# Performance work log

Measured on AMD Instinct MI355X. Metric: run time of the kernel, lower is better.

Reference implementation:

```python
import jax, jax.numpy as jnp
import numpy as np

N, L, E, H, D = 4, 2048, 1024, 16, 64

def setup_inputs() -> dict:
    key = jax.random.key(0)
    ks = jax.random.split(key, 8)
    s = 1.0 / np.sqrt(E)
    return {
        "Q": jax.random.normal(ks[0], (N, L, E), jnp.float32),
        "K": jax.random.normal(ks[1], (N, L, E), jnp.float32),
        "V": jax.random.normal(ks[2], (N, L, E), jnp.float32),
        "Wq": jax.random.normal(ks[3], (H * D, E), jnp.float32) * s,
        "bq": jnp.zeros((H * D,), jnp.float32),
        "Wk": jax.random.normal(ks[4], (H * D, E), jnp.float32) * s,
        "bk": jnp.zeros((H * D,), jnp.float32),
        "Wv": jax.random.normal(ks[5], (H * D, E), jnp.float32) * s,
        "bv": jnp.zeros((H * D,), jnp.float32),
        "Wo": jax.random.normal(ks[6], (E, H * D), jnp.float32) * s,
        "bo": jnp.zeros((E,), jnp.float32),
    }

def reference(Q, K, V, Wq, bq, Wk, bk, Wv, bv, Wo, bo):
    n, lq, e = Q.shape
    lk = K.shape[1]
    # projections: Linear(x) = x @ W.T + b
    q = (Q @ Wq.T + bq).reshape(n, lq, H, D)
    k = (K @ Wk.T + bk).reshape(n, lk, H, D)
    v = (V @ Wv.T + bv).reshape(n, lk, H, D)
    # scores over key dim (original broadcasts Q*K and sums over d)
    scores = jnp.einsum('nqhd,nkhd->nqkh', q, k) / jnp.sqrt(jnp.float32(D))
    attn = jax.nn.softmax(scores, axis=2)  # softmax over key axis
    out = jnp.einsum('nqkh,nkhd->nqhd', attn, v)
    out = out.reshape(n, lq, H * D)
    return (out @ Wo.T + bo).reshape(n, lq, E)
```

## Files before the change

kernel.cpp:

```cpp
#include <hip/hip_runtime.h>
#include <cstdint>
#include <cstddef>


typedef __bf16 bf16x8 __attribute__((ext_vector_type(8)));
typedef __bf16 bf16x4 __attribute__((ext_vector_type(4)));
typedef float f32x4 __attribute__((ext_vector_type(4)));

#define LOG2E_OVER_SQRTD 0.18033688011112042f

__device__ __forceinline__ unsigned short f2bf(float f) {
  unsigned int u = __builtin_bit_cast(unsigned int, f);
  u = (u + 0x7fffu + ((u >> 16) & 1u)) >> 16;
  return (unsigned short)u;
}

__device__ __forceinline__ void gl2lds16(const void* g, void* l) {
  __builtin_amdgcn_global_load_lds(
      (__attribute__((address_space(1))) unsigned int*)g,
      (__attribute__((address_space(3))) unsigned int*)l, 16, 0, 0);
}

struct CvtArgs {
  const float* src[4];
  unsigned short* dst[4];
};
__global__ __launch_bounds__(256) void cvt_multi_k(CvtArgs a) {
  const float* s = a.src[blockIdx.y];
  unsigned short* d = a.dst[blockIdx.y];
  size_t i = ((size_t)blockIdx.x * 256 + threadIdx.x) * 4;
  float4 v = *(const float4*)(s + i);
  ushort4 o;
  o.x = f2bf(v.x); o.y = f2bf(v.y); o.z = f2bf(v.z); o.w = f2bf(v.w);
  *(ushort4*)(d + i) = o;
}

template <bool OUT_F32, bool BIAS_ROW, bool PERMC>
__global__ __launch_bounds__(256, 2) void gemm_bt_k(
    const unsigned short* __restrict__ A, const unsigned short* __restrict__ Bt,
    const float* __restrict__ bias, void* __restrict__ Cv, int M, int N,
    float out_scale) {
  __shared__ __attribute__((aligned(16))) unsigned short As[128 * 32];
  __shared__ __attribute__((aligned(16))) unsigned short Bs[128 * 32];
  const int tid = threadIdx.x;
  const int lane = tid & 63, wave = tid >> 6;
  const int lr = lane & 15, lg = lane >> 4;
  const int rowBase = blockIdx.y * 128;
  const int colBase = blockIdx.x * 128;
  const int wm = (wave & 1) * 64, wn = (wave >> 1) * 64;

  f32x4 acc[4][4] = {};

  const int s0 = tid, s1 = tid + 256;
  const int r0 = s0 >> 2, c0 = (s0 & 3) ^ ((r0 >> 1) & 3);
  const int r1 = s1 >> 2, c1 = (s1 & 3) ^ ((r1 >> 1) & 3);
  const unsigned short* gA0 = A + (size_t)(rowBase + r0) * 1024 + c0 * 8;
  const unsigned short* gA1 = A + (size_t)(rowBase + r1) * 1024 + c1 * 8;
  const unsigned short* gB0 = Bt + (size_t)(colBase + r0) * 1024 + c0 * 8;
  const unsigned short* gB1 = Bt + (size_t)(colBase + r1) * 1024 + c1 * 8;
  unsigned short* lA0 = &As[s0 * 8];
  unsigned short* lA1 = &As[s1 * 8];
  unsigned short* lB0 = &Bs[s0 * 8];
  unsigned short* lB1 = &Bs[s1 * 8];

  for (int kt = 0; kt < 32; ++kt) {
    gl2lds16(gA0 + kt * 32, lA0);
    gl2lds16(gA1 + kt * 32, lA1);
    gl2lds16(gB0 + kt * 32, lB0);
    gl2lds16(gB1 + kt * 32, lB1);
    __syncthreads();

    bf16x8 af[4], bfr[4];
#pragma unroll
    for (int mt = 0; mt < 4; ++mt) {
      int row = wm + mt * 16 + lr;
      int seg = lg ^ ((row >> 1) & 3);
      af[mt] = *(const bf16x8*)&As[row * 32 + seg * 8];
    }
#pragma unroll
    for (int nt = 0; nt < 4; ++nt) {
      int row = wn + nt * 16 + lr;
      int seg = lg ^ ((row >> 1) & 3);
      bfr[nt] = *(const bf16x8*)&Bs[row * 32 + seg * 8];
    }
#pragma unroll
    for (int mt = 0; mt < 4; ++mt)
#pragma unroll
      for (int nt = 0; nt < 4; ++nt)
        acc[mt][nt] = __builtin_amdgcn_mfma_f32_16x16x32_bf16(
            af[mt], bfr[nt], acc[mt][nt], 0, 0, 0);
    __syncthreads();
  }

#pragma unroll
  for (int mt = 0; mt < 4; ++mt)
#pragma unroll
    for (int nt = 0; nt < 4; ++nt) {
      int col = colBase + wn + nt * 16 + lr;
      int colStore = PERMC ? (colBase + wn + lr * 4 + nt) : col;
      float bcol = BIAS_ROW ? 0.f : bias[col];
#pragma unroll
      for (int r = 0; r < 4; ++r) {
        int row = rowBase + wm + mt * 16 + lg * 4 + r;
        float b = BIAS_ROW ? bias[row] : bcol;
        float val = (acc[mt][nt][r] + b) * out_scale;
        size_t idx = (size_t)row * (size_t)N + (size_t)colStore;
        if (OUT_F32)
          ((float*)Cv)[idx] = val;
        else
          ((unsigned short*)Cv)[idx] = f2bf(val);
      }
    }
}

__global__ __launch_bounds__(256, 4) void attn_k(
    const unsigned short* __restrict__ qb,
    const unsigned short* __restrict__ kb,
    const unsigned short* __restrict__ vtb,
    unsigned short* __restrict__ aob) {
  __shared__ __attribute__((aligned(16))) unsigned short Ks[64 * 64];
  __shared__ __attribute__((aligned(16))) unsigned short Vts[64 * 64];
  __shared__ __attribute__((aligned(16))) unsigned short QPs[4 * 32 * 72];

  const int tid = threadIdx.x;
  const int lane = tid & 63, wave = tid >> 6;
  const int lr = lane & 15, lg = lane >> 4;

  const int bid = blockIdx.x;
  const int qt = bid & 15;
  const int nh = bid >> 4;
  const int h = nh & 15, n = nh >> 4;
  const int q0 = qt * 128;

#pragma unroll
  for (int i = 0; i < 4; ++i) {
    int s = i * 256 + tid;
    int row = s >> 3;
    int c = (s & 7) ^ (row & 7);
    gl2lds16(qb + (((size_t)n * 2048 + q0 + row) << 10) + h * 64 + c * 8,
             &QPs[s * 8]);
  }
#pragma unroll
  for (int i = 0; i < 2; ++i) {
    int s = i * 256 + tid;
    int row = s >> 3;
    int c = (s & 7) ^ (row & 7);
    gl2lds16(kb + (((size_t)n * 2048 + row) << 10) + h * 64 + c * 8, &Ks[s * 8]);
    gl2lds16(vtb + (((size_t)(h * 64 + row)) << 13) + (size_t)n * 2048 + c * 8,
             &Vts[s * 8]);
  }
  __syncthreads();

  bf16x8 aq[2][2];
#pragma unroll
  for (int mt = 0; mt < 2; ++mt)
#pragma unroll
    for (int ks = 0; ks < 2; ++ks) {
      int row = wave * 32 + mt * 16 + lr;
      int c = (ks * 4 + lg) ^ (row & 7);
      aq[mt][ks] = *(const bf16x8*)&QPs[row * 64 + c * 8];
    }
  __syncthreads();

  unsigned short* PsW = &QPs[wave * (32 * 72)];

  f32x4 o_acc[2][4] = {};
  float lrow[2][4] = {};

  for (int kt = 0; kt < 32; ++kt) {
    f32x4 s_acc[2][4] = {};
#pragma unroll
    for (int ks = 0; ks < 2; ++ks)
#pragma unroll
      for (int nt = 0; nt < 4; ++nt) {
        int row = nt * 16 + lr;
        int c = (ks * 4 + lg) ^ (row & 7);
        bf16x8 bk = *(const bf16x8*)&Ks[row * 64 + c * 8];
#pragma unroll
        for (int mt = 0; mt < 2; ++mt)
          s_acc[mt][nt] = __builtin_amdgcn_mfma_f32_16x16x32_bf16(
              aq[mt][ks], bk, s_acc[mt][nt], 0, 0, 0);
      }

#pragma unroll
    for (int mt = 0; mt < 2; ++mt) {
      f32x4 p[4];
#pragma unroll
      for (int nt = 0; nt < 4; ++nt)
#pragma unroll
        for (int r = 0; r < 4; ++r)
          p[nt][r] = __builtin_amdgcn_exp2f(s_acc[mt][nt][r]);
#pragma unroll
      for (int r = 0; r < 4; ++r) {
        lrow[mt][r] += (p[0][r] + p[1][r]) + (p[2][r] + p[3][r]);
        f32x4 v4 = {p[0][r], p[1][r], p[2][r], p[3][r]};
        bf16x4 pk = __builtin_convertvector(v4, bf16x4);
        int prow = mt * 16 + lg * 4 + r;
        *(bf16x4*)&PsW[prow * 72 + lr * 4] = pk;
      }
    }

#pragma unroll
    for (int ks = 0; ks < 2; ++ks) {
      bf16x8 ap[2], bv[4];
#pragma unroll
      for (int mt = 0; mt < 2; ++mt)
        ap[mt] = *(const bf16x8*)&PsW[(mt * 16 + lr) * 72 + ks * 32 + lg * 8];
#pragma unroll
      for (int nt = 0; nt < 4; ++nt) {
        int row = nt * 16 + lr;
        int c = (ks * 4 + lg) ^ (row & 7);
        bv[nt] = *(const bf16x8*)&Vts[row * 64 + c * 8];
      }
#pragma unroll
      for (int mt = 0; mt < 2; ++mt)
#pragma unroll
        for (int nt = 0; nt < 4; ++nt)
          o_acc[mt][nt] = __builtin_amdgcn_mfma_f32_16x16x32_bf16(
              ap[mt], bv[nt], o_acc[mt][nt], 0, 0, 0);
    }

    __syncthreads();
    if (kt < 31) {
      const int k0 = (kt + 1) * 64;
#pragma unroll
      for (int i = 0; i < 2; ++i) {
        int s = i * 256 + tid;
        int row = s >> 3;
        int c = (s & 7) ^ (row & 7);
        gl2lds16(kb + (((size_t)n * 2048 + k0 + row) << 10) + h * 64 + c * 8,
                 &Ks[s * 8]);
        gl2lds16(vtb + (((size_t)(h * 64 + row)) << 13) + (size_t)n * 2048 +
                     k0 + c * 8,
                 &Vts[s * 8]);
      }
    }
    __syncthreads();
  }

#pragma unroll
  for (int mt = 0; mt < 2; ++mt)
#pragma unroll
    for (int r = 0; r < 4; ++r) {
      float l = lrow[mt][r];
      l += __shfl_xor(l, 1);
      l += __shfl_xor(l, 2);
      l += __shfl_xor(l, 4);
      l += __shfl_xor(l, 8);
      float inv = 1.0f / l;
      int row_l = q0 + wave * 32 + mt * 16 + lg * 4 + r;
      size_t base = (((size_t)n * 2048 + row_l) << 10) + h * 64;
#pragma unroll
      for (int nt = 0; nt < 4; ++nt)
        aob[base + nt * 16 + lr] = f2bf(o_acc[mt][nt][r] * inv);
    }
}

extern "C" void kernel_launch(void* const* d_in, const int* in_sizes, int n_in,
                              void* d_out, int out_size, void* d_ws,
                              size_t ws_size, hipStream_t stream) {
  const float* Q = (const float*)d_in[0];
  const float* K = (const float*)d_in[1];
  const float* V = (const float*)d_in[2];
  const float* Wq = (const float*)d_in[3];
  const float* bq = (const float*)d_in[4];
  const float* Wk = (const float*)d_in[5];
  const float* bk = (const float*)d_in[6];
  const float* Wv = (const float*)d_in[7];
  const float* bv = (const float*)d_in[8];
  const float* Wo = (const float*)d_in[9];
  const float* bo = (const float*)d_in[10];

  const size_t S = (size_t)8192 * 1024;
  const size_t W = (size_t)1024 * 1024;
  unsigned short* ws = (unsigned short*)d_ws;
  unsigned short* Qbf = ws;
  unsigned short* Kbf = ws + S;
  unsigned short* Vbf = ws + 2 * S;
  unsigned short* qbuf = ws + 3 * S;
  unsigned short* kbuf = ws + 4 * S;
  unsigned short* vtbuf = ws + 5 * S;
  unsigned short* Wqb = ws + 6 * S;
  unsigned short* Wkb = Wqb + W;
  unsigned short* Wvb = Wqb + 2 * W;
  unsigned short* Wob = Wqb + 3 * W;
  unsigned short* aob = Qbf;

  CvtArgs cx;
  cx.src[0] = Q; cx.dst[0] = Qbf;
  cx.src[1] = K; cx.dst[1] = Kbf;
  cx.src[2] = V; cx.dst[2] = Vbf;
  cx.src[3] = Q; cx.dst[3] = Qbf;
  cvt_multi_k<<<dim3(8192, 3), 256, 0, stream>>>(cx);

  CvtArgs cw;
  cw.src[0] = Wq; cw.dst[0] = Wqb;
  cw.src[1] = Wk; cw.dst[1] = Wkb;
  cw.src[2] = Wv; cw.dst[2] = Wvb;
  cw.src[3] = Wo; cw.dst[3] = Wob;
  cvt_multi_k<<<dim3(1024, 4), 256, 0, stream>>>(cw);

  gemm_bt_k<false, false, false><<<dim3(8, 64), 256, 0, stream>>>(
      Qbf, Wqb, bq, qbuf, 8192, 1024, LOG2E_OVER_SQRTD);
  gemm_bt_k<false, false, false><<<dim3(8, 64), 256, 0, stream>>>(
      Kbf, Wkb, bk, kbuf, 8192, 1024, 1.0f);
  gemm_bt_k<false, true, true><<<dim3(64, 8), 256, 0, stream>>>(
      Wvb, Vbf, bv, vtbuf, 1024, 8192, 1.0f);

  attn_k<<<1024, 256, 0, stream>>>(qbuf, kbuf, vtbuf, aob);

  gemm_bt_k<true, false, false><<<dim3(8, 64), 256, 0, stream>>>(
      aob, Wob, bo, d_out, 8192, 1024, 1.0f);
}
```

Measured before the change: 353.5 us.

## Batch Q/K/V projection GEMMs into one launch and deepen K tile to 64

Merges the three projection GEMMs into a single grouped launch of 1536 blocks, with a descriptor table picking the operands for each block. This lets the three GEMMs fill the GPU together and removes per-launch tail effects. The K tile per iteration grows from 32 to 64, which halves the number of barrier-synchronised loads and uses an 8-way XOR swizzle. In exchange, LDS per block doubles to 32KB, and bias/permute choices become runtime branches instead of template specialisations.

```diff
diff --git a/kernel.cpp b/kernel.cpp
--- a/kernel.cpp
+++ b/kernel.cpp
@@ -35,60 +35,85 @@
   *(ushort4*)(d + i) = o;
 }
 
-template <bool OUT_F32, bool BIAS_ROW, bool PERMC>
-__global__ __launch_bounds__(256, 2) void gemm_bt_k(
-    const unsigned short* __restrict__ A, const unsigned short* __restrict__ Bt,
-    const float* __restrict__ bias, void* __restrict__ Cv, int M, int N,
-    float out_scale) {
-  __shared__ __attribute__((aligned(16))) unsigned short As[128 * 32];
-  __shared__ __attribute__((aligned(16))) unsigned short Bs[128 * 32];
+struct GemmDesc {
+  const unsigned short* A;
+  const unsigned short* Bt;
+  const float* bias;
+  void* C;
+  int N;
+  int nbx_shift;
+  float scale;
+  int bias_row;
+  int permc;
+};
+struct GemmPack3 {
+  GemmDesc g[3];
+};
+
+template <bool OUT_F32>
+__global__ __launch_bounds__(256, 2) void gemm_multi_k(GemmPack3 p) {
+  __shared__ __attribute__((aligned(16))) unsigned short As[128 * 64];
+  __shared__ __attribute__((aligned(16))) unsigned short Bs[128 * 64];
+  const GemmDesc d = p.g[blockIdx.x >> 9];
+  const int t = blockIdx.x & 511;
+  const int bx = t & ((1 << d.nbx_shift) - 1);
+  const int by = t >> d.nbx_shift;
+
   const int tid = threadIdx.x;
   const int lane = tid & 63, wave = tid >> 6;
   const int lr = lane & 15, lg = lane >> 4;
-  const int rowBase = blockIdx.y * 128;
-  const int colBase = blockIdx.x * 128;
+  const int rowBase = by * 128;
+  const int colBase = bx * 128;
   const int wm = (wave & 1) * 64, wn = (wave >> 1) * 64;
 
   f32x4 acc[4][4] = {};
 
-  const int s0 = tid, s1 = tid + 256;
-  const int r0 = s0 >> 2, c0 = (s0 & 3) ^ ((r0 >> 1) & 3);
-  const int r1 = s1 >> 2, c1 = (s1 & 3) ^ ((r1 >> 1) & 3);
-  const unsigned short* gA0 = A + (size_t)(rowBase + r0) * 1024 + c0 * 8;
-  const unsigned short* gA1 = A + (size_t)(rowBase + r1) * 1024 + c1 * 8;
-  const unsigned short* gB0 = Bt + (size_t)(colBase + r0) * 1024 + c0 * 8;
-  const unsigned short* gB1 = Bt + (size_t)(colBase + r1) * 1024 + c1 * 8;
-  unsigned short* lA0 = &As[s0 * 8];
-  unsigned short* lA1 = &As[s1 * 8];
-  unsigned short* lB0 = &Bs[s0 * 8];
-  unsigned short* lB1 = &Bs[s1 * 8];
-
-  for (int kt = 0; kt < 32; ++kt) {
-    gl2lds16(gA0 + kt * 32, lA0);
-    gl2lds16(gA1 + kt * 32, lA1);
-    gl2lds16(gB0 + kt * 32, lB0);
-    gl2lds16(gB1 + kt * 32, lB1);
+  const unsigned short* gA[4];
+  const unsigned short* gB[4];
+  unsigned short* lA[4];
+  unsigned short* lB[4];
+#pragma unroll
+  for (int i = 0; i < 4; ++i) {
+    int s = tid + i * 256;
+    int row = s >> 3;
+    int c = (s & 7) ^ (row & 7);
+    gA[i] = d.A + (size_t)(rowBase + row) * 1024 + c * 8;
+    gB[i] = d.Bt + (size_t)(colBase + row) * 1024 + c * 8;
+    lA[i] = &As[s * 8];
+    lB[i] = &Bs[s * 8];
+  }
+
+  for (int kt = 0; kt < 16; ++kt) {
+    const int ko = kt * 64;
+#pragma unroll
+    for (int i = 0; i < 4; ++i) {
+      gl2lds16(gA[i] + ko, lA[i]);
+      gl2lds16(gB[i] + ko, lB[i]);
+    }
     __syncthreads();
 
-    bf16x8 af[4], bfr[4];
-#pragma unroll
-    for (int mt = 0; mt < 4; ++mt) {
-      int row = wm + mt * 16 + lr;
-      int seg = lg ^ ((row >> 1) & 3);
-      af[mt] = *(const bf16x8*)&As[row * 32 + seg * 8];
-    }
-#pragma unroll
-    for (int nt = 0; nt < 4; ++nt) {
-      int row = wn + nt * 16 + lr;
-      int seg = lg ^ ((row >> 1) & 3);
-      bfr[nt] = *(const bf16x8*)&Bs[row * 32 + seg * 8];
-    }
-#pragma unroll
-    for (int mt = 0; mt < 4; ++mt)
-#pragma unroll
-      for (int nt = 0; nt < 4; ++nt)
-        acc[mt][nt] = __builtin_amdgcn_mfma_f32_16x16x32_bf16(
-            af[mt], bfr[nt], acc[mt][nt], 0, 0, 0);
+#pragma unroll
+    for (int ks = 0; ks < 2; ++ks) {
+      bf16x8 af[4], bfr[4];
+#pragma unroll
+      for (int mt = 0; mt < 4; ++mt) {
+        int row = wm + mt * 16 + lr;
+        int c = (ks * 4 + lg) ^ (row & 7);
+        af[mt] = *(const bf16x8*)&As[row * 64 + c * 8];
+      }
+#pragma unroll
+      for (int nt = 0; nt < 4; ++nt) {
+        int row = wn + nt * 16 + lr;
+        int c = (ks * 4 + lg) ^ (row & 7);
+        bfr[nt] = *(const bf16x8*)&Bs[row * 64 + c * 8];
+      }
+#pragma unroll
+      for (int mt = 0; mt < 4; ++mt)
+#pragma unroll
+        for (int nt = 0; nt < 4; ++nt)
+          acc[mt][nt] = __builtin_amdgcn_mfma_f32_16x16x32_bf16(
+              af[mt], bfr[nt], acc[mt][nt], 0, 0, 0);
+    }
     __syncthreads();
   }
 
@@ -97,18 +122,18 @@
 #pragma unroll
     for (int nt = 0; nt < 4; ++nt) {
       int col = colBase + wn + nt * 16 + lr;
-      int colStore = PERMC ? (colBase + wn + lr * 4 + nt) : col;
-      float bcol = BIAS_ROW ? 0.f : bias[col];
+      int colStore = d.permc ? (colBase + wn + lr * 4 + nt) : col;
+      float bcol = d.bias_row ? 0.f : d.bias[col];
 #pragma unroll
       for (int r = 0; r < 4; ++r) {
         int row = rowBase + wm + mt * 16 + lg * 4 + r;
-        float b = BIAS_ROW ? bias[row] : bcol;
-        float val = (acc[mt][nt][r] + b) * out_scale;
-        size_t idx = (size_t)row * (size_t)N + (size_t)colStore;
+        float b = d.bias_row ? d.bias[row] : bcol;
+        float val = (acc[mt][nt][r] + b) * d.scale;
+        size_t idx = (size_t)row * (size_t)d.N + (size_t)colStore;
         if (OUT_F32)
-          ((float*)Cv)[idx] = val;
+          ((float*)d.C)[idx] = val;
         else
-          ((unsigned short*)Cv)[idx] = f2bf(val);
+          ((unsigned short*)d.C)[idx] = f2bf(val);
       }
     }
 }
@@ -300,15 +325,17 @@
   cw.src[3] = Wo; cw.dst[3] = Wob;
   cvt_multi_k<<<dim3(1024, 4), 256, 0, stream>>>(cw);
 
-  gemm_bt_k<false, false, false><<<dim3(8, 64), 256, 0, stream>>>(
-      Qbf, Wqb, bq, qbuf, 8192, 1024, LOG2E_OVER_SQRTD);
-  gemm_bt_k<false, false, false><<<dim3(8, 64), 256, 0, stream>>>(
-      Kbf, Wkb, bk, kbuf, 8192, 1024, 1.0f);
-  gemm_bt_k<false, true, true><<<dim3(64, 8), 256, 0, stream>>>(
-      Wvb, Vbf, bv, vtbuf, 1024, 8192, 1.0f);
+  GemmPack3 pp;
+  pp.g[0] = {Qbf, Wqb, bq, qbuf, 1024, 3, LOG2E_OVER_SQRTD, 0, 0};
+  pp.g[1] = {Kbf, Wkb, bk, kbuf, 1024, 3, 1.0f, 0, 0};
+  pp.g[2] = {Wvb, Vbf, bv, vtbuf, 8192, 6, 1.0f, 1, 1};
+  gemm_multi_k<false><<<1536, 256, 0, stream>>>(pp);
 
   attn_k<<<1024, 256, 0, stream>>>(qbuf, kbuf, vtbuf, aob);
 
-  gemm_bt_k<true, false, false><<<dim3(8, 64), 256, 0, stream>>>(
-      aob, Wob, bo, d_out, 8192, 1024, 1.0f);
-}
+  GemmPack3 po;
+  po.g[0] = {aob, Wob, bo, d_out, 1024, 3, 1.0f, 0, 0};
+  po.g[1] = po.g[0];
+  po.g[2] = po.g[0];
+  gemm_multi_k<true><<<512, 256, 0, stream>>>(po);
+}
```

New measurement: 347.0 us. Within noise of the previous version (-1.9%).
